# Kernel tuning notes

Measured on AMD Instinct MI355X. Metric: run time of the kernel, lower is better.

## Reference

```python
import jax, jax.numpy as jnp
import numpy as np

RAD2DEG = 180.0 / 3.14159  # module uses 3.14159, not pi

def _conv2d(x, w):
    # x: (N,1,H,W), w: (O,1,3,3), SAME padding, stride 1
    return jax.lax.conv_general_dilated(
        x, w, window_strides=(1, 1), padding='SAME',
        dimension_numbers=('NCHW', 'OIHW', 'NCHW'))

def _make_filters():
    sobel = np.array([[1, 0, -1], [2, 0, -2], [1, 0, -1]], dtype=np.float32)
    f0   = [[0,0,0],[0,1,-1],[0,0,0]]
    f45  = [[0,0,0],[0,1,0],[0,0,-1]]
    f90  = [[0,0,0],[0,1,0],[0,-1,0]]
    f135 = [[0,0,0],[0,1,0],[-1,0,0]]
    f180 = [[0,0,0],[-1,1,0],[0,0,0]]
    f225 = [[-1,0,0],[0,1,0],[0,0,0]]
    f270 = [[0,-1,0],[0,1,0],[0,0,0]]
    f315 = [[0,0,-1],[0,1,0],[0,0,0]]
    dirs = np.stack([f0,f45,f90,f135,f180,f225,f270,f315]).astype(np.float32)
    return sobel, dirs

def setup_inputs() -> dict:
    key = jax.random.key(0)
    H, W = 2160, 3840
    img = jax.random.uniform(key, (1, 3, H, W), dtype=jnp.float32)
    sobel, dirs = _make_filters()
    sobel_h = jnp.asarray(sobel)[None, None]          # (1,1,3,3)
    sobel_v = jnp.asarray(sobel.T)[None, None]        # (1,1,3,3)
    dir_w = jnp.asarray(dirs)[:, None]                # (8,1,3,3)
    return {"img": img, "sobel_h": sobel_h, "sobel_v": sobel_v, "dir_w": dir_w}

def reference(img, sobel_h, sobel_v, dir_w):
    # grayscale: mean of the 3 channels
    gray = (img[:, 0:1] + img[:, 1:2] + img[:, 2:3]) / 3.0        # (1,1,H,W)
    grad_x = _conv2d(gray, sobel_h)
    grad_y = _conv2d(gray, sobel_v)
    grad_mag = jnp.sqrt(grad_x ** 2 + grad_y ** 2)                # (1,1,H,W)
    # orientation in degrees, snapped to multiples of 45 (round-half-even, like torch.round)
    ori = jnp.round((jnp.arctan2(grad_y, grad_x) * RAD2DEG + 180.0) / 45.0)
    idx_pos = jnp.mod(ori, 8.0).astype(jnp.int32)                 # (1,1,H,W)
    idx_neg = jnp.mod(ori + 4.0, 8.0).astype(jnp.int32)
    all_filtered = _conv2d(grad_mag, dir_w)                       # (1,8,H,W)
    # per-pixel channel select (the flattened gather in the original)
    pos = jnp.take_along_axis(all_filtered, idx_pos, axis=1)      # (1,1,H,W)
    neg = jnp.take_along_axis(all_filtered, idx_neg, axis=1)
    is_max = jnp.minimum(pos, neg) > 0.0
    # in-place aliasing in the original: thin_edges/early_threshold alias grad_mag,
    # so the final binary map is: is_max AND (grad_mag >= 0.2)
    th = jnp.where(is_max & (grad_mag >= 0.2), 1.0, 0.0).astype(jnp.float32)
    return th
```

## Files before the change

### kernel.cpp

```cpp
#include <hip/hip_runtime.h>
#include <math.h>

#define IMG_W 3840
#define IMG_H 2160
#define OUTW  60
#define R     20
#define GROWS (R + 4)

#define DXPACK 0x901A
#define DYPACK 0x1A9

#define T1_SLOPE 0.41421317376456f
#define T2_SLOPE 2.41420676743300f
#define SECT_EPS 3.0e-5f

__device__ __noinline__ int slow_sector(float sx, float sy) {
#pragma clang fp contract(off)
    const float RADF = (float)(180.0 / 3.14159);
    float t = atan2f(sy, sx);
    float wv = ((t * RADF) + 180.0f) / 45.0f;
    float ori = rintf(wv);
    float fr = fabsf(wv - ori);
    if (fr > 0.4995f) {
        double td = atan2((double)sy, (double)sx);
        float t2 = (float)td;
        wv = ((t2 * RADF) + 180.0f) / 45.0f;
        ori = rintf(wv);
    }
    return ((int)ori) & 7;
}


#define LOADROW(kk, cj)                                                        \
    {                                                                          \
        const int y_  = Y0 - 2 + (kk);                                         \
        const int yc_ = min(max(y_, 0), IMG_H - 1);                            \
        const int o_  = yc_ * IMG_W + xc;                                      \
        c0[(cj)] = img[o_];                                                    \
        c1[(cj)] = im1[o_];                                                    \
        c2[(cj)] = im2[o_];                                                    \
    }

#define GRAY(kk, j3)                                                           \
    {                                                                          \
        const int  y_   = Y0 - 2 + (kk);                                       \
        const bool yok_ = (unsigned)y_ < (unsigned)IMG_H;                      \
        float t_  = ((c0[(j3)] + c1[(j3)]) + c2[(j3)]) / 3.0f;                 \
        float gv_ = (xok && yok_) ? t_ : 0.0f;                                 \
        g[(j3)]  = gv_;                                                        \
        gl[(j3)] = __shfl_up(gv_, 1);                                          \
        gr[(j3)] = __shfl_down(gv_, 1);                                        \
    }

#define MAGROW(kk, j3, DONMS)                                                  \
    {                                                                          \
        const int i0_ = ((j3) + 2) & 3, i1_ = ((j3) + 3) & 3, i2_ = (j3);      \
        float a00 = gl[i0_], a01 = g[i0_], a02 = gr[i0_];                      \
        float a10 = gl[i1_],               a12 = gr[i1_];                      \
        float a20 = gl[i2_], a21 = g[i2_], a22 = gr[i2_];                      \
        float sx = a00;                                \
        sx = sx - a02;                                                         \
        sx = sx + 2.0f * a10;                                                  \
        sx = sx - 2.0f * a12;                                                  \
        sx = sx + a20;                                                         \
        sx = sx - a22;                                                         \
        float sy = a00;                                                        \
        sy = sy + 2.0f * a01;                                                  \
        sy = sy + a02;                                                         \
        sy = sy - a20;                                                         \
        sy = sy - 2.0f * a21;                                                  \
        sy = sy - a22;                                                         \
        float magv = sqrtf(sx * sx + sy * sy);                                 \
        float ax = fabsf(sx), ay = fabsf(sy);                                  \
        float d1 = fmaf(-T1_SLOPE, ax, ay);                                    \
        float d2 = fmaf(-T2_SLOPE, ax, ay);                                    \
        float sA = ax + ay;                                                    \
        int dxo, dyo;                                                          \
        if (__builtin_expect(fabsf(d1) < SECT_EPS * sA ||                      \
                             fabsf(d2) < SECT_EPS * sA, 0)) {                  \
            int idx = slow_sector(sx, sy);                                     \
            dxo = ((DXPACK >> (2 * idx)) & 3) - 1;                             \
            dyo = ((DYPACK >> (2 * idx)) & 3) - 1;                             \
        } else {                                                               \
            dxo = (d2 > 0.0f) ? 0 : ((sx > 0.0f) ? -1 : 1);                    \
            dyo = (d1 < 0.0f) ? 0 : ((sy > 0.0f) ? -1 : 1);                    \
        }                                                                      \
        const bool vok_ = xmok && ((unsigned)(Y0 - 3 + (kk)) < (unsigned)IMG_H); \
        float mag_  = vok_ ? magv : 0.0f;                                      \
        int   offv_ = vok_ ? (dyo * 64 + dxo) : 0;                             \
        B[(((j3) + 2) & 3) * 64 + lane] = mag_;    \
        if (DONMS) {                                                           \
            \
            const int rp_  = (((j3) + 1) & 3) * 64;                            \
            const int ipp_ = (rp_ + lane + off_p) & 255;                       \
            const int ipn_ = (rp_ + lane - off_p) & 255;                       \
            float mp_ = B[ipp_];                                               \
            float mn_ = B[ipn_];                                               \
            float res_ = (fminf(mc_p - mp_, mc_p - mn_) > 0.0f &&              \
                          mc_p >= 0.2f) ? 1.0f : 0.0f;                         \
            if (xoutok)                                                        \
                out[(size_t)(Y0 + (kk) - 4) * IMG_W + x] = res_;               \
        }                                                                      \
        mc_p  = mag_;                                                          \
        off_p = offv_;                                                         \
    }

__global__ __launch_bounds__(256, 4) void canny_like_kernel(const float* __restrict__ img,
                                                            float* __restrict__ out) {
#pragma clang fp contract(off)
    __shared__ float lds_m[4][4][64];

    const int lane = threadIdx.x;
    const int w    = threadIdx.y;
    const int X0   = (blockIdx.x * 4 + w) * OUTW;
    const int Y0   = blockIdx.y * R;
    const int x    = X0 - 2 + lane;
    const bool xok    = (unsigned)x < (unsigned)IMG_W;
    const int  xc     = min(max(x, 0), IMG_W - 1);
    const bool xmok   = (lane >= 1) && (lane <= 62) && xok;
    const bool xoutok = (lane >= 2) && (lane <= 61);

    const float* im1 = img + (size_t)IMG_W * IMG_H;
    const float* im2 = img + 2 * (size_t)IMG_W * IMG_H;

    float* const B = &lds_m[w][0][0];

    float c0[4], c1[4], c2[4];
    float g[4], gl[4], gr[4];
    float mc_p  = 0.0f;
    int   off_p = 0;

    LOADROW(0, 0)
    LOADROW(1, 1)
    LOADROW(2, 2)
    GRAY(0, 0)  LOADROW(3, 3)
    GRAY(1, 1)  LOADROW(4, 0)
    GRAY(2, 2)  LOADROW(5, 1)  MAGROW(2, 2, 0)
    GRAY(3, 3)  LOADROW(6, 2)  MAGROW(3, 3, 0)

#pragma clang loop unroll(disable)
    for (int kb = 4; kb < GROWS; kb += 4) {
        {   const int k_ = kb + 0;
            LOADROW(k_ + 3, 3)
            GRAY(k_, 0)
            MAGROW(k_, 0, 1)
        }
        {   const int k_ = kb + 1;
            LOADROW(k_ + 3, 0)
            GRAY(k_, 1)
            MAGROW(k_, 1, 1)
        }
        {   const int k_ = kb + 2;
            LOADROW(k_ + 3, 1)
            GRAY(k_, 2)
            MAGROW(k_, 2, 1)
        }
        {   const int k_ = kb + 3;
            LOADROW(k_ + 3, 2)
            GRAY(k_, 3)
            MAGROW(k_, 3, 1)
        }
    }
}

extern "C" void kernel_launch(void* const* d_in, const int* in_sizes, int n_in,
                              void* d_out, int out_size, void* d_ws, size_t ws_size,
                              hipStream_t stream) {
    const float* img = (const float*)d_in[0];
    float* out = (float*)d_out;
    dim3 grid(64 / 4, IMG_H / R);
    dim3 block(64, 4);
    canny_like_kernel<<<grid, block, 0, stream>>>(img, out);
}
```

Measured before the change: 166.3 us.

## Shrink row strip and fully unroll with deeper 8-row load prefetch

Cuts rows per block from 20 to 12, which doubles the grid in y. The loop becomes straight-line code that prefetches 8 input rows ahead instead of 3, so each thread keeps more loads in flight. The cost is more halo rows re-read per output row (4 extra per 12 instead of per 20) and higher register pressure from the 8-deep buffers.

```diff
diff --git a/kernel.cpp b/kernel.cpp
--- a/kernel.cpp
+++ b/kernel.cpp
@@ -4,7 +4,7 @@
 #define IMG_W 3840
 #define IMG_H 2160
 #define OUTW  60
-#define R     20
+#define R     12
 #define GROWS (R + 4)
 
 #define DXPACK 0x901A
@@ -41,11 +41,11 @@
         c2[(cj)] = im2[o_];                                                    \
     }
 
-#define GRAY(kk, j3)                                                           \
+#define GRAY(kk, cj, j3)                                                       \
     {                                                                          \
         const int  y_   = Y0 - 2 + (kk);                                       \
         const bool yok_ = (unsigned)y_ < (unsigned)IMG_H;                      \
-        float t_  = ((c0[(j3)] + c1[(j3)]) + c2[(j3)]) / 3.0f;                 \
+        float t_  = ((c0[(cj)] + c1[(cj)]) + c2[(cj)]) / 3.0f;                 \
         float gv_ = (xok && yok_) ? t_ : 0.0f;                                 \
         g[(j3)]  = gv_;                                                        \
         gl[(j3)] = __shfl_up(gv_, 1);                                          \
@@ -125,42 +125,31 @@
 
     float* const B = &lds_m[w][0][0];
 
-    float c0[4], c1[4], c2[4];
+    float c0[8], c1[8], c2[8];
     float g[4], gl[4], gr[4];
     float mc_p  = 0.0f;
     int   off_p = 0;
 
-    LOADROW(0, 0)
-    LOADROW(1, 1)
-    LOADROW(2, 2)
-    GRAY(0, 0)  LOADROW(3, 3)
-    GRAY(1, 1)  LOADROW(4, 0)
-    GRAY(2, 2)  LOADROW(5, 1)  MAGROW(2, 2, 0)
-    GRAY(3, 3)  LOADROW(6, 2)  MAGROW(3, 3, 0)
+    LOADROW(0, 0)  LOADROW(1, 1)  LOADROW(2, 2)  LOADROW(3, 3)
+    LOADROW(4, 4)  LOADROW(5, 5)  LOADROW(6, 6)  LOADROW(7, 7)
 
-#pragma clang loop unroll(disable)
-    for (int kb = 4; kb < GROWS; kb += 4) {
-        {   const int k_ = kb + 0;
-            LOADROW(k_ + 3, 3)
-            GRAY(k_, 0)
-            MAGROW(k_, 0, 1)
-        }
-        {   const int k_ = kb + 1;
-            LOADROW(k_ + 3, 0)
-            GRAY(k_, 1)
-            MAGROW(k_, 1, 1)
-        }
-        {   const int k_ = kb + 2;
-            LOADROW(k_ + 3, 1)
-            GRAY(k_, 2)
-            MAGROW(k_, 2, 1)
-        }
-        {   const int k_ = kb + 3;
-            LOADROW(k_ + 3, 2)
-            GRAY(k_, 3)
-            MAGROW(k_, 3, 1)
-        }
-    }
+    GRAY(0, 0, 0)  LOADROW( 8, 0)
+    GRAY(1, 1, 1)  LOADROW( 9, 1)
+    GRAY(2, 2, 2)  LOADROW(10, 2)  MAGROW(2, 2, 0)
+    GRAY(3, 3, 3)  LOADROW(11, 3)  MAGROW(3, 3, 0)
+    GRAY(4, 4, 0)  LOADROW(12, 4)  MAGROW(4, 0, 1)
+    GRAY(5, 5, 1)  LOADROW(13, 5)  MAGROW(5, 1, 1)
+    GRAY(6, 6, 2)  LOADROW(14, 6)  MAGROW(6, 2, 1)
+    GRAY(7, 7, 3)  LOADROW(15, 7)  MAGROW(7, 3, 1)
+
+    GRAY( 8, 0, 0)  MAGROW( 8, 0, 1)
+    GRAY( 9, 1, 1)  MAGROW( 9, 1, 1)
+    GRAY(10, 2, 2)  MAGROW(10, 2, 1)
+    GRAY(11, 3, 3)  MAGROW(11, 3, 1)
+    GRAY(12, 4, 0)  MAGROW(12, 0, 1)
+    GRAY(13, 5, 1)  MAGROW(13, 1, 1)
+    GRAY(14, 6, 2)  MAGROW(14, 2, 1)
+    GRAY(15, 7, 3)  MAGROW(15, 3, 1)
 }
 
 extern "C" void kernel_launch(void* const* d_in, const int* in_sizes, int n_in,
```

Measured after the change: 163.3 us. Within noise of the previous version (-1.8%).
